# Kernel optimization log

Hardware: AMD Instinct MI355X
Metric: run time of the kernel (lower is better)

Reference implementation:

```python
import jax, jax.numpy as jnp
import numpy as np

D_DISP = 20   # module arg d
S1 = 1        # module arg s1
WIN = D_DISP + S1


def setup_inputs() -> dict:
    key = jax.random.key(0)
    k1, k2 = jax.random.split(key)
    x1 = jax.random.normal(k1, (4, 128, 128, 128), dtype=jnp.float32)
    x2 = jax.random.normal(k2, (4, 128, 128, 128), dtype=jnp.float32)
    return {"x1": x1, "x2": x2}


def reference(x1, x2):
    b, c, w, h = x1.shape
    pad = D_DISP // 2
    # original code calls .detach() on the unfolded x2 patches
    x2p = jax.lax.stop_gradient(
        jnp.pad(x2, ((0, 0), (0, 0), (pad, pad), (pad, pad)))
    )  # [b, c, w+2*pad, h+2*pad]

    uv = jnp.arange(WIN * WIN)

    def step(carry, uv_i):
        u = uv_i // WIN
        v = uv_i % WIN
        win = jax.lax.dynamic_slice(x2p, (0, 0, u, v), (b, c, w, h))
        return carry, jnp.sum(x1 * win, axis=1)  # [b, w, h]

    _, out = jax.lax.scan(step, None, uv)
    return jnp.transpose(out, (1, 0, 2, 3))
```

## Files before the change

kernel.cpp:

```cpp
#include <hip/hip_runtime.h>

#define BATCH 4
#define CH    128
#define HW    128
#define PAD   10
#define PW    148
#define PWC   160
#define WIN   21
#define NUV   441
#define NQ    36

typedef short s16x8 __attribute__((ext_vector_type(8)));
typedef float f32x4 __attribute__((ext_vector_type(4)));
typedef unsigned short u16x8 __attribute__((ext_vector_type(8)));

static __device__ __forceinline__ unsigned short f32_to_bf16(float f) {
    unsigned int u = __float_as_uint(f);
    u += 0x7FFFu + ((u >> 16) & 1u);
    return (unsigned short)(u >> 16);
}

__global__ __launch_bounds__(256) void corr_transpose_kernel(
    const float* __restrict__ x1, const float* __restrict__ x2,
    unsigned short* __restrict__ x1b, unsigned short* __restrict__ x2b)
{
    __shared__ float lds[128][33];
    int bidx  = blockIdx.x;
    int which = bidx >= 2048;
    if (which) bidx -= 2048;
    int jt = bidx & 3;
    int i  = (bidx >> 2) & 127;
    int b  = bidx >> 9;
    int j0 = jt * 32;
    int t  = threadIdx.x;

    const float* __restrict__ src = which ? x2 : x1;

    int cl = t >> 3, jq = t & 7;
    #pragma unroll
    for (int it = 0; it < 4; ++it) {
        int c = it * 32 + cl;
        float4 vv = *(const float4*)&src[(((size_t)b * CH + c) * HW + i) * HW + j0 + jq * 4];
        lds[c][jq * 4 + 0] = vv.x;
        lds[c][jq * 4 + 1] = vv.y;
        lds[c][jq * 4 + 2] = vv.z;
        lds[c][jq * 4 + 3] = vv.w;
    }
    __syncthreads();

    int jl = t >> 4, cg = t & 15;
    #pragma unroll
    for (int it = 0; it < 2; ++it) {
        int j = it * 16 + jl;
        u16x8 o;
        #pragma unroll
        for (int k = 0; k < 8; ++k) o[k] = f32_to_bf16(lds[cg * 8 + k][j]);
        if (!which)
            *(u16x8*)&x1b[(((size_t)b * HW + i) * HW + j0 + j) * CH + cg * 8] = o;
        else
            *(u16x8*)&x2b[(((size_t)b * PW + i + PAD) * PWC + (j0 + j + PAD)) * CH + cg * 8] = o;
    }
}

__global__ __launch_bounds__(256, 3) void corr_mfma_kernel(
    const unsigned short* __restrict__ x1b,
    const unsigned short* __restrict__ x2b,
    float* __restrict__ out)
{
    __shared__ unsigned short ldsA[64 * 128];
    __shared__ unsigned short ldsB[4 * NQ * 128];

    int bid  = blockIdx.x;
    int swz  = (bid & 7) * 768 + (bid >> 3);
    int z    = swz % 6;
    int rest = swz / 6;
    int tj   = rest & 7;
    int ti   = (rest >> 3) & 31;
    int b    = rest >> 8;
    int i0 = ti * 4, j0 = tj * 16;

    int t    = threadIdx.x;
    int lane = t & 63;
    int w    = t >> 6;
    int l15  = lane & 15;
    int lhi  = lane >> 4;
    int rr   = z * 4 + w;

    #pragma unroll
    for (int it = 0; it < 4; ++it) {
        int s   = w * 4 + it;
        int dpi = s >> 2;
        int pl  = lane >> 4;
        int hs  = lane & 15;
        int p   = s * 4 + pl;
        int dpj = (s & 3) * 4 + pl;
        int h   = hs ^ (p & 7);
        const unsigned short* srcp =
            x1b + (((size_t)b * HW + i0 + dpi) * HW + j0 + dpj) * CH + h * 8;
        __builtin_amdgcn_global_load_lds(
            (const __attribute__((address_space(1))) void*)srcp,
            (__attribute__((address_space(3))) void*)(ldsA + s * 512),
            16, 0, 0);
    }

    const unsigned short* rowbase =
        x2b + (((size_t)b * PW + i0 + rr) * PWC + j0) * CH;
    unsigned short* myB = ldsB + w * (NQ * 128);
    #pragma unroll
    for (int g = 0; g < 9; ++g) {
        int ql = lane >> 4;
        int hs = lane & 15;
        int q  = g * 4 + ql;
        int h  = hs ^ (q & 7);
        const unsigned short* srcp = rowbase + (size_t)q * CH + h * 8;
        __builtin_amdgcn_global_load_lds(
            (const __attribute__((address_space(1))) void*)srcp,
            (__attribute__((address_space(3))) void*)(myB + g * 512),
            16, 0, 0);
    }

    __syncthreads();

    f32x4 acc[3][4];
    #pragma unroll
    for (int ntl = 0; ntl < 3; ++ntl)
        #pragma unroll
        for (int mt = 0; mt < 4; ++mt)
            acc[ntl][mt] = (f32x4)(0.0f);

    const int q0tab[3] = {0, 16, 20};

    #pragma unroll
    for (int kc = 0; kc < 4; ++kc) {
        s16x8 a[4], bb[3];
        #pragma unroll
        for (int mt = 0; mt < 4; ++mt) {
            int slot = (kc * 4 + lhi) ^ (l15 & 7);
            a[mt] = *(const s16x8*)(ldsA + (mt * 16 + l15) * 128 + slot * 8);
        }
        #pragma unroll
        for (int ntl = 0; ntl < 3; ++ntl) {
            int q    = q0tab[ntl] + l15;
            int slot = (kc * 4 + lhi) ^ (q & 7);
            bb[ntl] = *(const s16x8*)(myB + q * 128 + slot * 8);
        }
        __builtin_amdgcn_s_setprio(1);
        #pragma unroll
        for (int ntl = 0; ntl < 3; ++ntl)
            #pragma unroll
            for (int mt = 0; mt < 4; ++mt)
                acc[ntl][mt] = __builtin_amdgcn_mfma_f32_16x16x32_bf16(a[mt], bb[ntl], acc[ntl][mt], 0, 0, 0);
        __builtin_amdgcn_s_setprio(0);
    }

    float (*myCT)[20] = (float(*)[20])myB;
    #pragma unroll
    for (int dpi = 0; dpi < 4; ++dpi) {
        int u = rr - dpi;
        if ((unsigned)u < 21u) {
            int r2 = i0 + dpi + u - PAD;
            #pragma unroll
            for (int ntl = 0; ntl < 3; ++ntl)
                *(f32x4*)&myCT[q0tab[ntl] + l15][lhi * 4] = acc[ntl][dpi];
            #pragma unroll
            for (int vb = 0; vb < 6; ++vb) {
                int v = vb * 4 + lhi;
                if (v < 21) {
                    int c2 = j0 + l15 + v - PAD;
                    float val = myCT[l15 + v][l15];
                    if ((unsigned)r2 >= 128u || (unsigned)c2 >= 128u) val = 0.0f;
                    out[(((size_t)b * NUV + u * WIN + v) * HW + (i0 + dpi)) * HW + j0 + l15] = val;
                }
            }
        }
    }
}

extern "C" void kernel_launch(void* const* d_in, const int* in_sizes, int n_in,
                              void* d_out, int out_size, void* d_ws, size_t ws_size,
                              hipStream_t stream) {
    const float* x1 = (const float*)d_in[0];
    const float* x2 = (const float*)d_in[1];
    float* out = (float*)d_out;

    const size_t X1B_ELEMS = (size_t)BATCH * HW * HW * CH;
    const size_t X2B_ELEMS = (size_t)BATCH * PW * PWC * CH;
    if (ws_size < (X1B_ELEMS + X2B_ELEMS) * sizeof(unsigned short)) return;

    unsigned short* x1b = (unsigned short*)d_ws;
    unsigned short* x2b = x1b + X1B_ELEMS;

    corr_transpose_kernel<<<4096, 256, 0, stream>>>(x1, x2, x1b, x2b);
    corr_mfma_kernel<<<6144, 256, 0, stream>>>(x1b, x2b, out);
}
```

Before: 54.45 us.

## Fuse x1 bf16 transpose into MFMA kernel, load fp32 x1 directly into LDS

The separate transpose/convert pass for x1 is removed. The correlation kernel now reads fp32 x1 directly, converts it to bf16 and scatters it into the swizzled LDS tile. This drops one workspace write and read of x1 and halves the prep kernel's grid. In exchange, each of the 6 z-blocks sharing a tile re-reads fp32 x1 (twice the bytes of bf16), and the LDS stores become scalar 2-byte scattered writes instead of async global-to-LDS loads.

Result: slower. 58.54 us (+7.5%).

```diff
diff --git a/kernel.cpp b/kernel.cpp
--- a/kernel.cpp
+++ b/kernel.cpp
@@ -21,26 +21,21 @@
 }
 
 __global__ __launch_bounds__(256) void corr_transpose_kernel(
-    const float* __restrict__ x1, const float* __restrict__ x2,
-    unsigned short* __restrict__ x1b, unsigned short* __restrict__ x2b)
+    const float* __restrict__ x2, unsigned short* __restrict__ x2b)
 {
     __shared__ float lds[128][33];
-    int bidx  = blockIdx.x;
-    int which = bidx >= 2048;
-    if (which) bidx -= 2048;
+    int bidx = blockIdx.x;
     int jt = bidx & 3;
     int i  = (bidx >> 2) & 127;
     int b  = bidx >> 9;
     int j0 = jt * 32;
     int t  = threadIdx.x;
 
-    const float* __restrict__ src = which ? x2 : x1;
-
     int cl = t >> 3, jq = t & 7;
     #pragma unroll
     for (int it = 0; it < 4; ++it) {
         int c = it * 32 + cl;
-        float4 vv = *(const float4*)&src[(((size_t)b * CH + c) * HW + i) * HW + j0 + jq * 4];
+        float4 vv = *(const float4*)&x2[(((size_t)b * CH + c) * HW + i) * HW + j0 + jq * 4];
         lds[c][jq * 4 + 0] = vv.x;
         lds[c][jq * 4 + 1] = vv.y;
         lds[c][jq * 4 + 2] = vv.z;
@@ -55,15 +50,12 @@
         u16x8 o;
         #pragma unroll
         for (int k = 0; k < 8; ++k) o[k] = f32_to_bf16(lds[cg * 8 + k][j]);
-        if (!which)
-            *(u16x8*)&x1b[(((size_t)b * HW + i) * HW + j0 + j) * CH + cg * 8] = o;
-        else
-            *(u16x8*)&x2b[(((size_t)b * PW + i + PAD) * PWC + (j0 + j + PAD)) * CH + cg * 8] = o;
+        *(u16x8*)&x2b[(((size_t)b * PW + i + PAD) * PWC + (j0 + j + PAD)) * CH + cg * 8] = o;
     }
 }
 
 __global__ __launch_bounds__(256, 3) void corr_mfma_kernel(
-    const unsigned short* __restrict__ x1b,
+    const float* __restrict__ x1,
     const unsigned short* __restrict__ x2b,
     float* __restrict__ out)
 {
@@ -86,23 +78,6 @@
     int lhi  = lane >> 4;
     int rr   = z * 4 + w;
 
-    #pragma unroll
-    for (int it = 0; it < 4; ++it) {
-        int s   = w * 4 + it;
-        int dpi = s >> 2;
-        int pl  = lane >> 4;
-        int hs  = lane & 15;
-        int p   = s * 4 + pl;
-        int dpj = (s & 3) * 4 + pl;
-        int h   = hs ^ (p & 7);
-        const unsigned short* srcp =
-            x1b + (((size_t)b * HW + i0 + dpi) * HW + j0 + dpj) * CH + h * 8;
-        __builtin_amdgcn_global_load_lds(
-            (const __attribute__((address_space(1))) void*)srcp,
-            (__attribute__((address_space(3))) void*)(ldsA + s * 512),
-            16, 0, 0);
-    }
-
     const unsigned short* rowbase =
         x2b + (((size_t)b * PW + i0 + rr) * PWC + j0) * CH;
     unsigned short* myB = ldsB + w * (NQ * 128);
@@ -117,6 +92,27 @@
             (const __attribute__((address_space(1))) void*)srcp,
             (__attribute__((address_space(3))) void*)(myB + g * 512),
             16, 0, 0);
+    }
+
+    {
+        int c16 = lane >> 2;
+        int j4  = lane & 3;
+        #pragma unroll
+        for (int it = 0; it < 8; ++it) {
+            int s   = w * 8 + it;
+            int dpi = s >> 3;
+            int cg  = s & 7;
+            int c   = cg * 16 + c16;
+            float4 vv = *(const float4*)&x1[(((size_t)b * CH + c) * HW + i0 + dpi) * HW + j0 + j4 * 4];
+            int h = c >> 3;
+            #pragma unroll
+            for (int jj = 0; jj < 4; ++jj) {
+                int p    = dpi * 16 + j4 * 4 + jj;
+                int slot = h ^ (p & 7);
+                float fv = (jj == 0) ? vv.x : (jj == 1) ? vv.y : (jj == 2) ? vv.z : vv.w;
+                ldsA[p * 128 + slot * 8 + (c16 & 7)] = f32_to_bf16(fv);
+            }
+        }
     }
 
     __syncthreads();
@@ -183,13 +179,11 @@
     const float* x2 = (const float*)d_in[1];
     float* out = (float*)d_out;
 
-    const size_t X1B_ELEMS = (size_t)BATCH * HW * HW * CH;
     const size_t X2B_ELEMS = (size_t)BATCH * PW * PWC * CH;
-    if (ws_size < (X1B_ELEMS + X2B_ELEMS) * sizeof(unsigned short)) return;
+    if (ws_size < X2B_ELEMS * sizeof(unsigned short)) return;
 
-    unsigned short* x1b = (unsigned short*)d_ws;
-    unsigned short* x2b = x1b + X1B_ELEMS;
+    unsigned short* x2b = (unsigned short*)d_ws;
 
-    corr_transpose_kernel<<<4096, 256, 0, stream>>>(x1, x2, x1b, x2b);
-    corr_mfma_kernel<<<6144, 256, 0, stream>>>(x1b, x2b, out);
+    corr_transpose_kernel<<<2048, 256, 0, stream>>>(x2, x2b);
+    corr_mfma_kernel<<<6144, 256, 0, stream>>>(x1, x2b, out);
 }
```

## Split B-tile channel loads into two halves to shrink LDS and raise occupancy

Applied to the files above, without the earlier changes.

Each wave's shifted x2 row tile is now loaded in two 64-channel phases into a half-size per-wave LDS buffer (40 positions by 64 channels) instead of one 36x128 buffer. The second half is fetched after the first two K-chunks finish, and the launch bound is raised from three to four blocks per CU. The goal is to cut LDS use per block so more blocks fit per CU and hide memory latency better. In exchange, each wave now stalls on a mid-kernel vmcnt(0) wait for the second load, and the rounded-up 40-position tile loads a few extra rows.

Result: no change. 53.42 us (-1.9%).

```diff
diff --git a/kernel.cpp b/kernel.cpp
--- a/kernel.cpp
+++ b/kernel.cpp
@@ -8,7 +8,7 @@
 #define PWC   160
 #define WIN   21
 #define NUV   441
-#define NQ    36
+#define NQS   40
 
 typedef short s16x8 __attribute__((ext_vector_type(8)));
 typedef float f32x4 __attribute__((ext_vector_type(4)));
@@ -62,13 +62,13 @@
     }
 }
 
-__global__ __launch_bounds__(256, 3) void corr_mfma_kernel(
+__global__ __launch_bounds__(256, 4) void corr_mfma_kernel(
     const unsigned short* __restrict__ x1b,
     const unsigned short* __restrict__ x2b,
     float* __restrict__ out)
 {
     __shared__ unsigned short ldsA[64 * 128];
-    __shared__ unsigned short ldsB[4 * NQ * 128];
+    __shared__ unsigned short ldsB[4 * NQS * 64];
 
     int bid  = blockIdx.x;
     int swz  = (bid & 7) * 768 + (bid >> 3);
@@ -85,6 +85,13 @@
     int l15  = lane & 15;
     int lhi  = lane >> 4;
     int rr   = z * 4 + w;
+
+    const unsigned short* rowbase =
+        x2b + (((size_t)b * PW + i0 + rr) * PWC + j0) * CH;
+    unsigned short* myB = ldsB + w * (NQS * 64);
+
+    int bq  = lane >> 3;
+    int bc2 = (lane & 7) ^ bq;
 
     #pragma unroll
     for (int it = 0; it < 4; ++it) {
@@ -103,16 +110,10 @@
             16, 0, 0);
     }
 
-    const unsigned short* rowbase =
-        x2b + (((size_t)b * PW + i0 + rr) * PWC + j0) * CH;
-    unsigned short* myB = ldsB + w * (NQ * 128);
-    #pragma unroll
-    for (int g = 0; g < 9; ++g) {
-        int ql = lane >> 4;
-        int hs = lane & 15;
-        int q  = g * 4 + ql;
-        int h  = hs ^ (q & 7);
-        const unsigned short* srcp = rowbase + (size_t)q * CH + h * 8;
+    #pragma unroll
+    for (int g = 0; g < 5; ++g) {
+        int q = g * 8 + bq;
+        const unsigned short* srcp = rowbase + (size_t)q * CH + bc2 * 8;
         __builtin_amdgcn_global_load_lds(
             (const __attribute__((address_space(1))) void*)srcp,
             (__attribute__((address_space(3))) void*)(myB + g * 512),
@@ -131,26 +132,45 @@
     const int q0tab[3] = {0, 16, 20};
 
     #pragma unroll
-    for (int kc = 0; kc < 4; ++kc) {
-        s16x8 a[4], bb[3];
-        #pragma unroll
-        for (int mt = 0; mt < 4; ++mt) {
-            int slot = (kc * 4 + lhi) ^ (l15 & 7);
-            a[mt] = *(const s16x8*)(ldsA + (mt * 16 + l15) * 128 + slot * 8);
+    for (int ph = 0; ph < 2; ++ph) {
+        if (ph == 1) {
+            asm volatile("s_waitcnt lgkmcnt(0)" ::: "memory");
+            __builtin_amdgcn_sched_barrier(0);
+            #pragma unroll
+            for (int g = 0; g < 5; ++g) {
+                int q = g * 8 + bq;
+                const unsigned short* srcp = rowbase + (size_t)q * CH + 64 + bc2 * 8;
+                __builtin_amdgcn_global_load_lds(
+                    (const __attribute__((address_space(1))) void*)srcp,
+                    (__attribute__((address_space(3))) void*)(myB + g * 512),
+                    16, 0, 0);
+            }
+            asm volatile("s_waitcnt vmcnt(0)" ::: "memory");
+            __builtin_amdgcn_sched_barrier(0);
         }
         #pragma unroll
-        for (int ntl = 0; ntl < 3; ++ntl) {
-            int q    = q0tab[ntl] + l15;
-            int slot = (kc * 4 + lhi) ^ (q & 7);
-            bb[ntl] = *(const s16x8*)(myB + q * 128 + slot * 8);
+        for (int kc2 = 0; kc2 < 2; ++kc2) {
+            int kc = ph * 2 + kc2;
+            s16x8 a[4], bb[3];
+            #pragma unroll
+            for (int mt = 0; mt < 4; ++mt) {
+                int slot = (kc * 4 + lhi) ^ (l15 & 7);
+                a[mt] = *(const s16x8*)(ldsA + (mt * 16 + l15) * 128 + slot * 8);
+            }
+            #pragma unroll
+            for (int ntl = 0; ntl < 3; ++ntl) {
+                int q    = q0tab[ntl] + l15;
+                int slot = (kc2 * 4 + lhi) ^ (q & 7);
+                bb[ntl] = *(const s16x8*)(myB + q * 64 + slot * 8);
+            }
+            __builtin_amdgcn_s_setprio(1);
+            #pragma unroll
+            for (int ntl = 0; ntl < 3; ++ntl)
+                #pragma unroll
+                for (int mt = 0; mt < 4; ++mt)
+                    acc[ntl][mt] = __builtin_amdgcn_mfma_f32_16x16x32_bf16(a[mt], bb[ntl], acc[ntl][mt], 0, 0, 0);
+            __builtin_amdgcn_s_setprio(0);
         }
-        __builtin_amdgcn_s_setprio(1);
-        #pragma unroll
-        for (int ntl = 0; ntl < 3; ++ntl)
-            #pragma unroll
-            for (int mt = 0; mt < 4; ++mt)
-                acc[ntl][mt] = __builtin_amdgcn_mfma_f32_16x16x32_bf16(a[mt], bb[ntl], acc[ntl][mt], 0, 0, 0);
-        __builtin_amdgcn_s_setprio(0);
     }
 
     float (*myCT)[20] = (float(*)[20])myB;
```

## Double-buffer x2 channel quarters per wave to overlap loads with MFMA and raise occupancy

Applied to the files above, without the earlier changes.

Each wave now stages its x2 row tile in two LDS buffers of 32 channels each, instead of loading all 128 channels up front. Loads for the next channel quarter are issued while MFMAs run on the current one, coordinated with explicit vmcnt waits and sched barriers. The smaller B buffer cuts LDS per block, so the launch bound rises to 4 blocks per CU, and the block barrier now waits only for the shared x1 tile. The risks are more wait points, a tighter register budget, and correctness relying on hand-tuned vmcnt counts.

New measurement: 54.97 us. No clear change (+0.9%).

```diff
diff --git a/kernel.cpp b/kernel.cpp
--- a/kernel.cpp
+++ b/kernel.cpp
@@ -8,7 +8,6 @@
 #define PWC   160
 #define WIN   21
 #define NUV   441
-#define NQ    36
 
 typedef short s16x8 __attribute__((ext_vector_type(8)));
 typedef float f32x4 __attribute__((ext_vector_type(4)));
@@ -62,13 +61,13 @@
     }
 }
 
-__global__ __launch_bounds__(256, 3) void corr_mfma_kernel(
+__global__ __launch_bounds__(256, 4) void corr_mfma_kernel(
     const unsigned short* __restrict__ x1b,
     const unsigned short* __restrict__ x2b,
     float* __restrict__ out)
 {
     __shared__ unsigned short ldsA[64 * 128];
-    __shared__ unsigned short ldsB[4 * NQ * 128];
+    __shared__ unsigned short ldsB[4 * 2 * 1536];
 
     int bid  = blockIdx.x;
     int swz  = (bid & 7) * 768 + (bid >> 3);
@@ -85,6 +84,26 @@
     int l15  = lane & 15;
     int lhi  = lane >> 4;
     int rr   = z * 4 + w;
+
+    const unsigned short* rowbase =
+        x2b + (((size_t)b * PW + i0 + rr) * PWC + j0) * CH;
+    unsigned short* buf0 = ldsB + (w * 2 + 0) * 1536;
+    unsigned short* buf1 = ldsB + (w * 2 + 1) * 1536;
+
+    int qs = lane >> 2;
+    int ck = lane & 3;
+    int hB = ck ^ (qs & 3);
+
+    #define ISSUE_QUARTER(buf, qt)                                                     \
+        _Pragma("unroll")                                                              \
+        for (int g = 0; g < 3; ++g) {                                                  \
+            const unsigned short* srcp =                                               \
+                rowbase + (size_t)(g * 16 + qs) * CH + (qt) * 32 + hB * 8;             \
+            __builtin_amdgcn_global_load_lds(                                          \
+                (const __attribute__((address_space(1))) void*)srcp,                   \
+                (__attribute__((address_space(3))) void*)((buf) + g * 512),            \
+                16, 0, 0);                                                             \
+        }
 
     #pragma unroll
     for (int it = 0; it < 4; ++it) {
@@ -102,24 +121,14 @@
             (__attribute__((address_space(3))) void*)(ldsA + s * 512),
             16, 0, 0);
     }
-
-    const unsigned short* rowbase =
-        x2b + (((size_t)b * PW + i0 + rr) * PWC + j0) * CH;
-    unsigned short* myB = ldsB + w * (NQ * 128);
-    #pragma unroll
-    for (int g = 0; g < 9; ++g) {
-        int ql = lane >> 4;
-        int hs = lane & 15;
-        int q  = g * 4 + ql;
-        int h  = hs ^ (q & 7);
-        const unsigned short* srcp = rowbase + (size_t)q * CH + h * 8;
-        __builtin_amdgcn_global_load_lds(
-            (const __attribute__((address_space(1))) void*)srcp,
-            (__attribute__((address_space(3))) void*)(myB + g * 512),
-            16, 0, 0);
-    }
-
-    __syncthreads();
+    ISSUE_QUARTER(buf0, 0)
+    ISSUE_QUARTER(buf1, 1)
+
+    __builtin_amdgcn_sched_barrier(0);
+    asm volatile("s_waitcnt vmcnt(6)" ::: "memory");
+    __builtin_amdgcn_sched_barrier(0);
+    __builtin_amdgcn_s_barrier();
+    __builtin_amdgcn_sched_barrier(0);
 
     f32x4 acc[3][4];
     #pragma unroll
@@ -130,30 +139,55 @@
 
     const int q0tab[3] = {0, 16, 20};
 
-    #pragma unroll
-    for (int kc = 0; kc < 4; ++kc) {
-        s16x8 a[4], bb[3];
-        #pragma unroll
-        for (int mt = 0; mt < 4; ++mt) {
-            int slot = (kc * 4 + lhi) ^ (l15 & 7);
-            a[mt] = *(const s16x8*)(ldsA + (mt * 16 + l15) * 128 + slot * 8);
+    #define KC_STEP(kc, buf)                                                           \
+        {                                                                              \
+            s16x8 a[4], bb[3];                                                         \
+            _Pragma("unroll")                                                          \
+            for (int mt = 0; mt < 4; ++mt) {                                           \
+                int slot = ((kc) * 4 + lhi) ^ (l15 & 7);                               \
+                a[mt] = *(const s16x8*)(ldsA + (mt * 16 + l15) * 128 + slot * 8);      \
+            }                                                                          \
+            _Pragma("unroll")                                                          \
+            for (int ntl = 0; ntl < 3; ++ntl) {                                        \
+                int q    = q0tab[ntl] + l15;                                           \
+                int slot = lhi ^ (q & 3);                                              \
+                bb[ntl] = *(const s16x8*)((buf) + q * 32 + slot * 8);                  \
+            }                                                                          \
+            __builtin_amdgcn_s_setprio(1);                                             \
+            _Pragma("unroll")                                                          \
+            for (int ntl = 0; ntl < 3; ++ntl)                                          \
+                _Pragma("unroll")                                                      \
+                for (int mt = 0; mt < 4; ++mt)                                         \
+                    acc[ntl][mt] = __builtin_amdgcn_mfma_f32_16x16x32_bf16(            \
+                        a[mt], bb[ntl], acc[ntl][mt], 0, 0, 0);                        \
+            __builtin_amdgcn_s_setprio(0);                                             \
         }
-        #pragma unroll
-        for (int ntl = 0; ntl < 3; ++ntl) {
-            int q    = q0tab[ntl] + l15;
-            int slot = (kc * 4 + lhi) ^ (q & 7);
-            bb[ntl] = *(const s16x8*)(myB + q * 128 + slot * 8);
-        }
-        __builtin_amdgcn_s_setprio(1);
-        #pragma unroll
-        for (int ntl = 0; ntl < 3; ++ntl)
-            #pragma unroll
-            for (int mt = 0; mt < 4; ++mt)
-                acc[ntl][mt] = __builtin_amdgcn_mfma_f32_16x16x32_bf16(a[mt], bb[ntl], acc[ntl][mt], 0, 0, 0);
-        __builtin_amdgcn_s_setprio(0);
-    }
-
-    float (*myCT)[20] = (float(*)[20])myB;
+
+    asm volatile("s_waitcnt vmcnt(3)" ::: "memory");
+    __builtin_amdgcn_sched_barrier(0);
+    KC_STEP(0, buf0)
+    __builtin_amdgcn_sched_barrier(0);
+
+    asm volatile("s_waitcnt vmcnt(0)" ::: "memory");
+    __builtin_amdgcn_sched_barrier(0);
+    ISSUE_QUARTER(buf0, 2)
+    __builtin_amdgcn_sched_barrier(0);
+
+    KC_STEP(1, buf1)
+    __builtin_amdgcn_sched_barrier(0);
+
+    ISSUE_QUARTER(buf1, 3)
+    __builtin_amdgcn_sched_barrier(0);
+    asm volatile("s_waitcnt vmcnt(3)" ::: "memory");
+    __builtin_amdgcn_sched_barrier(0);
+    KC_STEP(2, buf0)
+    __builtin_amdgcn_sched_barrier(0);
+
+    asm volatile("s_waitcnt vmcnt(0)" ::: "memory");
+    __builtin_amdgcn_sched_barrier(0);
+    KC_STEP(3, buf1)
+
+    float (*myCT)[20] = (float(*)[20])buf0;
     #pragma unroll
     for (int dpi = 0; dpi < 4; ++dpi) {
         int u = rr - dpi;
@@ -174,6 +208,8 @@
             }
         }
     }
+    #undef KC_STEP
+    #undef ISSUE_QUARTER
 }
 
 extern "C" void kernel_launch(void* const* d_in, const int* in_sizes, int n_in,
```
